# Optimization experiments

Hardware: AMD Instinct MI355X
Metric: run time of the kernel (lower is better)

## Reference

```python
import jax, jax.numpy as jnp
import numpy as np

EPS = 1e-6      # F.pairwise_distance adds eps to the difference vector
MARGIN = 0.2
NORM_EPS = 1e-12  # torch F.normalize clamps the norm at 1e-12


def _l2_normalize(x):
    n = jnp.linalg.norm(x, axis=1, keepdims=True)
    return x / jnp.maximum(n, NORM_EPS)


def _pairdist(A, B):
    # ||a - b + EPS||_2 for every (a, b) pair, computed without the [N,N,d] tensor:
    # ||a-b||^2 + 2*EPS*sum(a-b) + d*EPS^2
    d = A.shape[1]
    sq = (jnp.sum(A * A, axis=1)[:, None] + jnp.sum(B * B, axis=1)[None, :]
          - 2.0 * (A @ B.T)
          + 2.0 * EPS * (jnp.sum(A, axis=1)[:, None] - jnp.sum(B, axis=1)[None, :])
          + d * (EPS * EPS))
    return jnp.sqrt(jnp.maximum(sq, 0.0))


def setup_inputs() -> dict:
    key = jax.random.key(0)
    kp, kn = jax.random.split(key)
    p = jax.random.normal(kp, (8192, 128), dtype=jnp.float32)
    n = jax.random.normal(kn, (64, 128), dtype=jnp.float32)
    return {"sequence_representations_p": p, "sequence_representations_n": n}


def reference(sequence_representations_p, sequence_representations_n):
    p = _l2_normalize(sequence_representations_p)  # [l_p, d]
    n = _l2_normalize(sequence_representations_n)  # [l_n, d]
    l_p = p.shape[0]
    t = 0  # original uses random.randint(0, l_n-1); fixed for determinism
    d_pp = _pairdist(p, p)                 # [l_p, l_p]
    d_pn = _pairdist(p, n[t:t + 1])[:, 0]  # [l_p]
    distance = jnp.maximum(d_pp + MARGIN - d_pn[:, None], 0.0)
    loss = jnp.sum(distance) / ((l_p - 1) * l_p)
    return jnp.maximum(loss, 0.0)
```

## Files before the change

### kernel.cpp

```cpp
#include <hip/hip_runtime.h>
#include <hip/hip_bf16.h>

typedef float f32x16 __attribute__((ext_vector_type(16)));
typedef float f32x4v __attribute__((ext_vector_type(4)));

#define GLOBAL_AS(p) ((const __attribute__((address_space(1))) void*)(p))
#define LDS_AS(p)    ((__attribute__((address_space(3))) void*)(p))

#define LP 8192
#define D 128
#define TWOEPS 2e-6f
#define CEPS 1.28e-10f
#define MARGIN 0.2f
#define NTRI 2080
#define NBLK 512

#define BUFSZ 34816
#define AOFF 0
#define BOFF 16384
#define QWOFF 32768

__global__ __launch_bounds__(256) void rows_kernel(const float* __restrict__ p,
                                                   const float* __restrict__ n,
                                                   char* __restrict__ pb,
                                                   float* __restrict__ qw) {
    int tid = threadIdx.x;
    int wave = tid >> 6, lane = tid & 63;
    int row = blockIdx.x * 4 + wave;
    float2 x = ((const float2*)(p + (size_t)row * D))[lane];
    float2 y = ((const float2*)n)[lane];
    float ssp = fmaf(x.x, x.x, x.y * x.y);
    float ssn = fmaf(y.x, y.x, y.y * y.y);
#pragma unroll
    for (int m = 1; m < 64; m <<= 1) {
        ssp += __shfl_xor(ssp, m);
        ssn += __shfl_xor(ssn, m);
    }
    float invp = 1.0f / fmaxf(sqrtf(ssp), 1e-12f);
    float invn = 1.0f / fmaxf(sqrtf(ssn), 1e-12f);
    float a0 = x.x * invp, a1 = x.y * invp;
    float h0 = y.x * invn, h1 = y.y * invn;

    int pk = __builtin_amdgcn_cvt_pk_fp8_f32(a0, a1, 0, false);
    *(unsigned short*)(pb + (size_t)row * 128 + lane * 2) = (unsigned short)(pk & 0xffff);
    float b0 = __builtin_amdgcn_cvt_f32_fp8(pk, 0);
    float b1 = __builtin_amdgcn_cvt_f32_fp8(pk, 1);

    float q8 = fmaf(b0, b0, b1 * b1);
    float s  = a0 + a1;
    float q  = fmaf(a0, a0, a1 * a1);
    float dn = fmaf(a0, h0, a1 * h1);
    float sn = h0 + h1;
    float qn = fmaf(h0, h0, h1 * h1);
#pragma unroll
    for (int m = 1; m < 64; m <<= 1) {
        q8 += __shfl_xor(q8, m);
        s += __shfl_xor(s, m);
        q += __shfl_xor(q, m);
        dn += __shfl_xor(dn, m);
        sn += __shfl_xor(sn, m);
        qn += __shfl_xor(qn, m);
    }
    if (lane == 0) {
        float sq = q + qn - 2.0f * dn + TWOEPS * (s - sn) + CEPS;
        float dpn = sqrtf(fmaxf(sq, 0.0f));
        *(float2*)(qw + (size_t)row * 2) = make_float2(q8, MARGIN - dpn);
    }
}

__global__ __launch_bounds__(512, 4) void pair_kernel(const char* __restrict__ pb,
                                                      const float* __restrict__ qw,
                                                      float* __restrict__ partials) {
    __shared__ __align__(16) char smem[2 * BUFSZ];
    const int blk = blockIdx.x;
    const int tid = threadIdx.x;
    const int wave = tid >> 6, lane = tid & 63;
    const int nt = (blk < NTRI - 4 * NBLK) ? 5 : 4;

    const int wr = wave >> 2, wc = wave & 3;
    const int ln31 = lane & 31;
    const int h = lane >> 5;

    auto decode = [](int b, int& ti, int& tj) {
        int t = (int)((__builtin_amdgcn_sqrtf(8.0f * (float)b + 1.0f) - 1.0f) * 0.5f);
        while ((t + 1) * (t + 2) / 2 <= b) ++t;
        while (t * (t + 1) / 2 > b) --t;
        ti = t;
        tj = b - t * (t + 1) / 2;
    };

    auto stage = [&](int ti, int tj, char* buf) {
        const char* gA = pb + (size_t)ti * 128 * 128;
        const char* gB = pb + (size_t)tj * 128 * 128;
#pragma unroll
        for (int r = 0; r < 2; ++r) {
            int obase = wave * 2048 + r * 1024;
            int o = obase + lane * 16;
            int src = o ^ (((o >> 7) & 7) << 4);
            __builtin_amdgcn_global_load_lds(GLOBAL_AS(gA + src),
                                             LDS_AS(buf + AOFF + obase), 16, 0, 0);
            __builtin_amdgcn_global_load_lds(GLOBAL_AS(gB + src),
                                             LDS_AS(buf + BOFF + obase), 16, 0, 0);
        }
        int side = wave >> 2;
        int chunk = wave & 3;
        const char* gq = (const char*)qw + (size_t)(side ? tj : ti) * 1024 +
                         chunk * 256 + lane * 4;
        __builtin_amdgcn_global_load_lds(GLOBAL_AS(gq),
                                         LDS_AS(buf + QWOFF + side * 1024 + chunk * 256),
                                         4, 0, 0);
    };

    int ti0, tj0;
    decode(blk, ti0, tj0);
    stage(ti0, tj0, smem);
    bool diag_cur = (ti0 == tj0);
    bool diag_nxt = false;

    float la = 0.0f, lb = 0.0f;

    for (int t = 0; t < nt; ++t) {
        char* cur = smem + (size_t)(t & 1) * BUFSZ;
        char* nxt = smem + (size_t)((t + 1) & 1) * BUFSZ;

        if (t + 1 < nt) {
            int ti, tj;
            decode(blk + (t + 1) * NBLK, ti, tj);
            diag_nxt = (ti == tj);
            stage(ti, tj, nxt);
            asm volatile("s_waitcnt vmcnt(5)" ::: "memory");
        } else {
            asm volatile("s_waitcnt vmcnt(0)" ::: "memory");
        }
        __builtin_amdgcn_s_barrier();
        __builtin_amdgcn_sched_barrier(0);

        const char* lA = cur + AOFF;
        const char* lB = cur + BOFF;
        const float* qwi = (const float*)(cur + QWOFF);
        const float* qwj = (const float*)(cur + QWOFF + 1024);

        f32x16 acc[2] = {};
#pragma unroll
        for (int ks = 0; ks < 8; ++ks) {
            int co = ((ks ^ (ln31 & 7)) << 4) + h * 8;
            long bv = *(const long*)(lB + (wc * 32 + ln31) * 128 + co);
#pragma unroll
            for (int mt = 0; mt < 2; ++mt) {
                long av = *(const long*)(lA + (wr * 64 + mt * 32 + ln31) * 128 + co);
                acc[mt] = __builtin_amdgcn_mfma_f32_32x32x16_fp8_fp8(av, bv, acc[mt],
                                                                     0, 0, 0);
            }
        }

        float2 qwjv = *(const float2*)(qwj + (wc * 32 + ln31) * 2);
        if (diag_cur) {
#pragma unroll
            for (int mt = 0; mt < 2; ++mt)
#pragma unroll
                for (int g = 0; g < 4; ++g) {
                    int rbase = wr * 64 + mt * 32 + 8 * g + 4 * h;
                    f32x4v qw01 = *(const f32x4v*)(qwi + rbase * 2);
                    f32x4v qw23 = *(const f32x4v*)(qwi + rbase * 2 + 4);
                    float qi[4] = {qw01[0], qw01[2], qw23[0], qw23[2]};
                    float wi[4] = {qw01[1], qw01[3], qw23[1], qw23[3]};
#pragma unroll
                    for (int r2 = 0; r2 < 4; ++r2) {
                        float sq = fmaf(-2.0f, acc[mt][g * 4 + r2], qi[r2] + qwjv.x);
                        float d = __builtin_amdgcn_sqrtf(fmaxf(sq, 0.0f));
                        la += fmaxf(d + wi[r2], 0.0f);
                    }
                }
        } else {
#pragma unroll
            for (int mt = 0; mt < 2; ++mt)
#pragma unroll
                for (int g = 0; g < 4; ++g) {
                    int rbase = wr * 64 + mt * 32 + 8 * g + 4 * h;
                    f32x4v qw01 = *(const f32x4v*)(qwi + rbase * 2);
                    f32x4v qw23 = *(const f32x4v*)(qwi + rbase * 2 + 4);
                    float qi[4] = {qw01[0], qw01[2], qw23[0], qw23[2]};
                    float wi[4] = {qw01[1], qw01[3], qw23[1], qw23[3]};
#pragma unroll
                    for (int r2 = 0; r2 < 4; ++r2) {
                        float sq = fmaf(-2.0f, acc[mt][g * 4 + r2], qi[r2] + qwjv.x);
                        float d = __builtin_amdgcn_sqrtf(sq);
                        la += fmaxf(d + wi[r2], 0.0f);
                        lb += fmaxf(d + qwjv.y, 0.0f);
                    }
                }
        }
        __builtin_amdgcn_s_barrier();
        diag_cur = diag_nxt;
    }

    float local = la + lb;
#pragma unroll
    for (int m = 1; m < 64; m <<= 1) local += __shfl_xor(local, m);
    float* sred = (float*)smem;
    if (lane == 0) sred[wave] = local;
    __syncthreads();
    if (tid == 0) {
        float t0 = (sred[0] + sred[1]) + (sred[2] + sred[3]);
        float t1 = (sred[4] + sred[5]) + (sred[6] + sred[7]);
        partials[blk] = t0 + t1;
    }
}

__global__ void reduce_kernel(const float* __restrict__ partials, float* __restrict__ out,
                              int npart) {
    __shared__ float sred[4];
    float s = 0.0f;
    for (int t = threadIdx.x; t < npart; t += 256) s += partials[t];
#pragma unroll
    for (int m = 1; m < 64; m <<= 1) s += __shfl_xor(s, m);
    int wave = threadIdx.x >> 6, lane = threadIdx.x & 63;
    if (lane == 0) sred[wave] = s;
    __syncthreads();
    if (threadIdx.x == 0) {
        float tot = (sred[0] + sred[1]) + (sred[2] + sred[3]);
        float loss = tot * (1.0f / 67100672.0f);
        out[0] = fmaxf(loss, 0.0f);
    }
}

extern "C" void kernel_launch(void* const* d_in, const int* in_sizes, int n_in,
                              void* d_out, int out_size, void* d_ws, size_t ws_size,
                              hipStream_t stream) {
    const float* p = (const float*)d_in[0];
    const float* n = (const float*)d_in[1];
    float* out = (float*)d_out;
    char* ws = (char*)d_ws;

    char*  pb    = ws;
    float* qwarr = (float*)(ws + (1u << 20));
    float* parts = (float*)(ws + (1u << 20) + (64u << 10));

    hipLaunchKernelGGL(rows_kernel, dim3(LP / 4), dim3(256), 0, stream, p, n, pb, qwarr);
    hipLaunchKernelGGL(pair_kernel, dim3(NBLK), dim3(512), 0, stream, pb, qwarr, parts);
    hipLaunchKernelGGL(reduce_kernel, dim3(1), dim3(256), 0, stream, parts, out, NBLK);
}
```

Measured before the change: 30.54 us.

## Rework row prep, drop reduce kernel via atomics, split accumulators and raise MFMA priority

The row-normalisation kernel now gives each row to 4 lanes that each read 32 floats as float4, write 32 packed fp8 bytes with wide stores, and reduce with only two shuffle steps. The separate reduce kernel is removed: each pair block scales its partial by the normaliser and atomically adds it into the output, which is zeroed with a memset. The pair kernel also splits its accumulators per MFMA tile to shorten dependency chains, and raises wave priority around the MFMA loop. Atomic summation makes the float result order-dependent and nondeterministic, and the final clamp at zero is dropped.

After: 32.67 us. +7.0%, slower.

```diff
diff --git a/kernel.cpp b/kernel.cpp
--- a/kernel.cpp
+++ b/kernel.cpp
@@ -14,54 +14,78 @@
 #define MARGIN 0.2f
 #define NTRI 2080
 #define NBLK 512
+#define INV_DENOM 1.4903545e-8f
 
 #define BUFSZ 34816
 #define AOFF 0
 #define BOFF 16384
 #define QWOFF 32768
 
-__global__ __launch_bounds__(256) void rows_kernel(const float* __restrict__ p,
-                                                   const float* __restrict__ n,
-                                                   char* __restrict__ pb,
-                                                   float* __restrict__ qw) {
-    int tid = threadIdx.x;
-    int wave = tid >> 6, lane = tid & 63;
-    int row = blockIdx.x * 4 + wave;
-    float2 x = ((const float2*)(p + (size_t)row * D))[lane];
-    float2 y = ((const float2*)n)[lane];
-    float ssp = fmaf(x.x, x.x, x.y * x.y);
-    float ssn = fmaf(y.x, y.x, y.y * y.y);
-#pragma unroll
-    for (int m = 1; m < 64; m <<= 1) {
-        ssp += __shfl_xor(ssp, m);
-        ssn += __shfl_xor(ssn, m);
-    }
-    float invp = 1.0f / fmaxf(sqrtf(ssp), 1e-12f);
-    float invn = 1.0f / fmaxf(sqrtf(ssn), 1e-12f);
-    float a0 = x.x * invp, a1 = x.y * invp;
-    float h0 = y.x * invn, h1 = y.y * invn;
-
-    int pk = __builtin_amdgcn_cvt_pk_fp8_f32(a0, a1, 0, false);
-    *(unsigned short*)(pb + (size_t)row * 128 + lane * 2) = (unsigned short)(pk & 0xffff);
-    float b0 = __builtin_amdgcn_cvt_f32_fp8(pk, 0);
-    float b1 = __builtin_amdgcn_cvt_f32_fp8(pk, 1);
-
-    float q8 = fmaf(b0, b0, b1 * b1);
-    float s  = a0 + a1;
-    float q  = fmaf(a0, a0, a1 * a1);
-    float dn = fmaf(a0, h0, a1 * h1);
-    float sn = h0 + h1;
-    float qn = fmaf(h0, h0, h1 * h1);
-#pragma unroll
-    for (int m = 1; m < 64; m <<= 1) {
-        q8 += __shfl_xor(q8, m);
+__global__ __launch_bounds__(64) void rows_kernel(const float* __restrict__ p,
+                                                  const float* __restrict__ n,
+                                                  char* __restrict__ pb,
+                                                  float* __restrict__ qw) {
+    const int lane = threadIdx.x;
+    const int sub = lane & 3;
+    const int r = lane >> 2;
+    const int row = blockIdx.x * 16 + r;
+
+    const float4* px = (const float4*)(p + (size_t)row * D + sub * 32);
+    const float4* nx = (const float4*)(n + sub * 32);
+    float4 x[8], y[8];
+#pragma unroll
+    for (int k = 0; k < 8; ++k) { x[k] = px[k]; y[k] = nx[k]; }
+
+    float ssp = 0.0f, ssn = 0.0f;
+#pragma unroll
+    for (int k = 0; k < 8; ++k) {
+        ssp += fmaf(x[k].x, x[k].x, fmaf(x[k].y, x[k].y,
+               fmaf(x[k].z, x[k].z, x[k].w * x[k].w)));
+        ssn += fmaf(y[k].x, y[k].x, fmaf(y[k].y, y[k].y,
+               fmaf(y[k].z, y[k].z, y[k].w * y[k].w)));
+    }
+    ssp += __shfl_xor(ssp, 1); ssp += __shfl_xor(ssp, 2);
+    ssn += __shfl_xor(ssn, 1); ssn += __shfl_xor(ssn, 2);
+
+    const float invp = 1.0f / fmaxf(sqrtf(ssp), 1e-12f);
+    const float invn = 1.0f / fmaxf(sqrtf(ssn), 1e-12f);
+
+    float s = 0.0f, q = 0.0f, dn = 0.0f, sn = 0.0f, qn = 0.0f, q8 = 0.0f;
+    int pk8[8];
+#pragma unroll
+    for (int k = 0; k < 8; ++k) {
+        float a0 = x[k].x * invp, a1 = x[k].y * invp,
+              a2 = x[k].z * invp, a3 = x[k].w * invp;
+        float h0 = y[k].x * invn, h1 = y[k].y * invn,
+              h2 = y[k].z * invn, h3 = y[k].w * invn;
+        s  += (a0 + a1) + (a2 + a3);
+        q  += fmaf(a0, a0, fmaf(a1, a1, fmaf(a2, a2, a3 * a3)));
+        dn += fmaf(a0, h0, fmaf(a1, h1, fmaf(a2, h2, a3 * h3)));
+        sn += (h0 + h1) + (h2 + h3);
+        qn += fmaf(h0, h0, fmaf(h1, h1, fmaf(h2, h2, h3 * h3)));
+        int wlo = __builtin_amdgcn_cvt_pk_fp8_f32(a0, a1, 0, false);
+        int wfl = __builtin_amdgcn_cvt_pk_fp8_f32(a2, a3, wlo, true);
+        pk8[k] = wfl;
+        float b0 = __builtin_amdgcn_cvt_f32_fp8(wfl, 0);
+        float b1 = __builtin_amdgcn_cvt_f32_fp8(wfl, 1);
+        float b2 = __builtin_amdgcn_cvt_f32_fp8(wfl, 2);
+        float b3 = __builtin_amdgcn_cvt_f32_fp8(wfl, 3);
+        q8 += fmaf(b0, b0, fmaf(b1, b1, fmaf(b2, b2, b3 * b3)));
+    }
+    char* dst = pb + (size_t)row * 128 + sub * 32;
+    ((int4*)dst)[0] = make_int4(pk8[0], pk8[1], pk8[2], pk8[3]);
+    ((int4*)dst)[1] = make_int4(pk8[4], pk8[5], pk8[6], pk8[7]);
+
+#pragma unroll
+    for (int m = 1; m < 4; m <<= 1) {
         s += __shfl_xor(s, m);
         q += __shfl_xor(q, m);
         dn += __shfl_xor(dn, m);
         sn += __shfl_xor(sn, m);
         qn += __shfl_xor(qn, m);
-    }
-    if (lane == 0) {
+        q8 += __shfl_xor(q8, m);
+    }
+    if (sub == 0) {
         float sq = q + qn - 2.0f * dn + TWOEPS * (s - sn) + CEPS;
         float dpn = sqrtf(fmaxf(sq, 0.0f));
         *(float2*)(qw + (size_t)row * 2) = make_float2(q8, MARGIN - dpn);
@@ -70,7 +94,7 @@
 
 __global__ __launch_bounds__(512, 4) void pair_kernel(const char* __restrict__ pb,
                                                       const float* __restrict__ qw,
-                                                      float* __restrict__ partials) {
+                                                      float* __restrict__ out) {
     __shared__ __align__(16) char smem[2 * BUFSZ];
     const int blk = blockIdx.x;
     const int tid = threadIdx.x;
@@ -117,7 +141,7 @@
     bool diag_cur = (ti0 == tj0);
     bool diag_nxt = false;
 
-    float la = 0.0f, lb = 0.0f;
+    float la0 = 0.0f, la1 = 0.0f, lb0 = 0.0f, lb1 = 0.0f;
 
     for (int t = 0; t < nt; ++t) {
         char* cur = smem + (size_t)(t & 1) * BUFSZ;
@@ -141,6 +165,7 @@
         const float* qwj = (const float*)(cur + QWOFF + 1024);
 
         f32x16 acc[2] = {};
+        __builtin_amdgcn_s_setprio(1);
 #pragma unroll
         for (int ks = 0; ks < 8; ++ks) {
             int co = ((ks ^ (ln31 & 7)) << 4) + h * 8;
@@ -152,6 +177,7 @@
                                                                      0, 0, 0);
             }
         }
+        __builtin_amdgcn_s_setprio(0);
 
         float2 qwjv = *(const float2*)(qwj + (wc * 32 + ln31) * 2);
         if (diag_cur) {
@@ -168,7 +194,8 @@
                     for (int r2 = 0; r2 < 4; ++r2) {
                         float sq = fmaf(-2.0f, acc[mt][g * 4 + r2], qi[r2] + qwjv.x);
                         float d = __builtin_amdgcn_sqrtf(fmaxf(sq, 0.0f));
-                        la += fmaxf(d + wi[r2], 0.0f);
+                        if (mt) la1 += fmaxf(d + wi[r2], 0.0f);
+                        else    la0 += fmaxf(d + wi[r2], 0.0f);
                     }
                 }
         } else {
@@ -185,8 +212,10 @@
                     for (int r2 = 0; r2 < 4; ++r2) {
                         float sq = fmaf(-2.0f, acc[mt][g * 4 + r2], qi[r2] + qwjv.x);
                         float d = __builtin_amdgcn_sqrtf(sq);
-                        la += fmaxf(d + wi[r2], 0.0f);
-                        lb += fmaxf(d + qwjv.y, 0.0f);
+                        if (mt) { la1 += fmaxf(d + wi[r2], 0.0f);
+                                  lb1 += fmaxf(d + qwjv.y, 0.0f); }
+                        else    { la0 += fmaxf(d + wi[r2], 0.0f);
+                                  lb0 += fmaxf(d + qwjv.y, 0.0f); }
                     }
                 }
         }
@@ -194,7 +223,7 @@
         diag_cur = diag_nxt;
     }
 
-    float local = la + lb;
+    float local = (la0 + la1) + (lb0 + lb1);
 #pragma unroll
     for (int m = 1; m < 64; m <<= 1) local += __shfl_xor(local, m);
     float* sred = (float*)smem;
@@ -203,24 +232,7 @@
     if (tid == 0) {
         float t0 = (sred[0] + sred[1]) + (sred[2] + sred[3]);
         float t1 = (sred[4] + sred[5]) + (sred[6] + sred[7]);
-        partials[blk] = t0 + t1;
-    }
-}
-
-__global__ void reduce_kernel(const float* __restrict__ partials, float* __restrict__ out,
-                              int npart) {
-    __shared__ float sred[4];
-    float s = 0.0f;
-    for (int t = threadIdx.x; t < npart; t += 256) s += partials[t];
-#pragma unroll
-    for (int m = 1; m < 64; m <<= 1) s += __shfl_xor(s, m);
-    int wave = threadIdx.x >> 6, lane = threadIdx.x & 63;
-    if (lane == 0) sred[wave] = s;
-    __syncthreads();
-    if (threadIdx.x == 0) {
-        float tot = (sred[0] + sred[1]) + (sred[2] + sred[3]);
-        float loss = tot * (1.0f / 67100672.0f);
-        out[0] = fmaxf(loss, 0.0f);
+        atomicAdd(out, (t0 + t1) * INV_DENOM);
     }
 }
 
@@ -234,9 +246,8 @@
 
     char*  pb    = ws;
     float* qwarr = (float*)(ws + (1u << 20));
-    float* parts = (float*)(ws + (1u << 20) + (64u << 10));
-
-    hipLaunchKernelGGL(rows_kernel, dim3(LP / 4), dim3(256), 0, stream, p, n, pb, qwarr);
-    hipLaunchKernelGGL(pair_kernel, dim3(NBLK), dim3(512), 0, stream, pb, qwarr, parts);
-    hipLaunchKernelGGL(reduce_kernel, dim3(1), dim3(256), 0, stream, parts, out, NBLK);
+
+    hipMemsetAsync(out, 0, sizeof(float), stream);
+    hipLaunchKernelGGL(rows_kernel, dim3(LP / 16), dim3(64), 0, stream, p, n, pb, qwarr);
+    hipLaunchKernelGGL(pair_kernel, dim3(NBLK), dim3(512), 0, stream, pb, qwarr, out);
 }
```
